# Kernel optimization log

Hardware: AMD Instinct MI355X
Metric: run time of the kernel (lower is better)

The kernel has to match this reference:

```python
import jax, jax.numpy as jnp
from jax import lax
import numpy as np

I_CNN = 2048   # box feature dim
Q_H = 1024     # LSTM hidden
Q_E = 300      # word embedding dim
HID = 512      # gated MLP hidden
B = 256
MAXN = 100
T = 14


def setup_inputs() -> dict:
    key = jax.random.key(0)
    ks = jax.random.split(key, 12)
    w = lambda k, shape: (jax.random.normal(k, shape, dtype=jnp.float32) * 0.02)
    return {
        "wholefeat": jax.random.normal(ks[0], (B, I_CNN), dtype=jnp.float32),
        "pooled": jax.random.normal(ks[1], (B, I_CNN), dtype=jnp.float32),
        "box_feats": jax.random.normal(ks[2], (B, MAXN, I_CNN), dtype=jnp.float32),
        "q_feats": jax.random.normal(ks[3], (B, T, Q_E), dtype=jnp.float32),
        "box_coords": jax.random.uniform(ks[4], (B, MAXN, 4), dtype=jnp.float32),
        "index": jax.random.randint(ks[5], (B,), 1, MAXN + 1),
        # LSTM params (PyTorch layout: gates ordered i,f,g,o)
        "W_ih": w(ks[6], (4 * Q_H, Q_E)),
        "W_hh": w(ks[7], (4 * Q_H, Q_H)),
        "b_ih": jnp.zeros((4 * Q_H,), jnp.float32),
        "b_hh": jnp.zeros((4 * Q_H,), jnp.float32),
        # gated MLP params
        "W_w": w(ks[8], (HID, I_CNN + Q_H)),
        "W_b": jnp.zeros((HID,), jnp.float32),
        "Wp_w": w(ks[9], (HID, I_CNN + Q_H)),
        "Wp_b": jnp.zeros((HID,), jnp.float32),
        "f_w": w(ks[10], (1, HID)),
    }


def _lstm_last(x_tbe, W_ih, W_hh, b_ih, b_hh):
    # x_tbe: [T, B, E] time-major. Returns final hidden state h_T: [B, H].
    H = W_hh.shape[1]
    # precompute input projections for all timesteps: [T, B, 4H]
    xg = jnp.einsum('tbe,ge->tbg', x_tbe, W_ih) + (b_ih + b_hh)

    def step(carry, xt):
        h, c = carry
        gates = xt + h @ W_hh.T                       # [B, 4H]
        i, f, g, o = jnp.split(gates, 4, axis=-1)
        i = jax.nn.sigmoid(i)
        f = jax.nn.sigmoid(f)
        g = jnp.tanh(g)
        o = jax.nn.sigmoid(o)
        c = f * c + i * g
        h = o * jnp.tanh(c)
        return (h, c), None

    h0 = jnp.zeros((x_tbe.shape[1], H), x_tbe.dtype)
    (h, _), _ = lax.scan(step, (h0, h0), xg)
    return h


def reference(wholefeat, pooled, box_feats, q_feats, box_coords, index,
              W_ih, W_hh, b_ih, b_hh, W_w, W_b, Wp_w, Wp_b, f_w):
    # question encoding: last LSTM output per sample -> [B, Q_H]
    q_rnn = _lstm_last(jnp.transpose(q_feats, (1, 0, 2)), W_ih, W_hh, b_ih, b_hh)

    Bn, N, _ = box_feats.shape
    qst = jnp.broadcast_to(q_rnn[:, None, :], (Bn, N, q_rnn.shape[-1]))
    b_full = jnp.concatenate([box_feats, qst], axis=-1)        # [B, N, 3072]

    y_tilde = jnp.tanh(jnp.einsum('bnd,hd->bnh', b_full, W_w) + W_b)
    g = jax.nn.sigmoid(jnp.einsum('bnd,hd->bnh', b_full, Wp_w) + Wp_b)
    si = y_tilde * g                                           # [B, N, HID]
    wsi = jax.nn.sigmoid(jnp.einsum('bnh,oh->bno', si, f_w))[..., 0]  # [B, N]

    # ragged reduction: only the first index[i] boxes of sample i contribute
    mask = (jnp.arange(N)[None, :] < index[:, None]).astype(wsi.dtype)
    return jnp.sum(wsi * mask, axis=1)                         # [B]
```

## Files before the change

kernel.cpp:

```cpp
#include <hip/hip_runtime.h>
#include <cstdint>
#include <cstddef>

#define DEVI __device__ __forceinline__

typedef __attribute__((ext_vector_type(8))) short short8;
typedef __attribute__((ext_vector_type(4))) float f32x4;
typedef __bf16 bf16x8 __attribute__((ext_vector_type(8)));

DEVI float sigf(float x) { return 1.0f / (1.0f + __expf(-x)); }
DEVI float tanh_f(float x) { return 2.0f / (1.0f + __expf(-2.0f * x)) - 1.0f; }

DEVI short f2bf(float x) {
    uint32_t u = __builtin_bit_cast(uint32_t, x);
    u += 0x7FFFu + ((u >> 16) & 1u);
    return (short)(u >> 16);
}
DEVI float bf2f(short s) {
    uint32_t u = ((uint32_t)(unsigned short)s) << 16;
    return __builtin_bit_cast(float, u);
}

DEVI void gload16(const void* g, void* l) {
    __builtin_amdgcn_global_load_lds(
        (const __attribute__((address_space(1))) void*)g,
        (__attribute__((address_space(3))) void*)l, 16, 0, 0);
}

DEVI f32x4 mfma16(short8 a, short8 b, f32x4 c) {
    return __builtin_amdgcn_mfma_f32_16x16x32_bf16(
        __builtin_bit_cast(bf16x8, a), __builtin_bit_cast(bf16x8, b), c, 0, 0, 0);
}


#define W_SLOTS   688128
#define WC_SLOTS  393216
#define XB_SLOTS  143360
#define HB_SLOTS  32768
#define C_SLOTS   65536
#define LG_SLOTS  6400
#define PREP_TOT  (W_SLOTS + WC_SLOTS + XB_SLOTS + HB_SLOTS + C_SLOTS + LG_SLOTS)

__global__ __launch_bounds__(256) void prep_all(const float* __restrict__ Wih,
                                                const float* __restrict__ Whh,
                                                const float* __restrict__ bih,
                                                const float* __restrict__ bhh,
                                                const float* __restrict__ Ww,
                                                const float* __restrict__ Wpw,
                                                const float* __restrict__ q,
                                                short* __restrict__ Wstk,
                                                short* __restrict__ Wcat,
                                                short* __restrict__ xb,
                                                short* __restrict__ hb0,
                                                float* __restrict__ c,
                                                float* __restrict__ lgt) {
    int s = blockIdx.x * 256 + threadIdx.x;
    if (s < W_SLOTS) {
        int n = s / 168, c8 = s - n * 168, kb = c8 * 8;
        int hblk = n >> 6, gate = (n >> 4) & 3, hl = n & 15;
        int on = gate * 1024 + hblk * 16 + hl;
        short8 o;
#pragma unroll
        for (int e = 0; e < 8; ++e) {
            int k = kb + e;
            float v;
            if (k < 300) v = Wih[on * 300 + k];
            else if (k == 300) v = bih[on] + bhh[on];
            else if (k < 320) v = 0.f;
            else v = Whh[on * 1024 + (k - 320)];
            o[e] = f2bf(v);
        }
        *(short8*)&Wstk[n * 1344 + kb] = o;
        return;
    }
    s -= W_SLOTS;
    if (s < WC_SLOTS) {
        int n = s / 384, c8 = s - n * 384, kb = c8 * 8;
        int hg = n >> 5, which = (n >> 4) & 1, hl = n & 15;
        int h = hg * 16 + hl;
        const float* src = (which ? Wpw : Ww) + (size_t)h * 3072 + kb;
        float4 v0 = *(const float4*)src;
        float4 v1 = *(const float4*)(src + 4);
        short8 o;
        o[0] = f2bf(v0.x); o[1] = f2bf(v0.y); o[2] = f2bf(v0.z); o[3] = f2bf(v0.w);
        o[4] = f2bf(v1.x); o[5] = f2bf(v1.y); o[6] = f2bf(v1.z); o[7] = f2bf(v1.w);
        *(short8*)&Wcat[(size_t)n * 3072 + kb] = o;
        return;
    }
    s -= WC_SLOTS;
    if (s < XB_SLOTS) {
        int row = s / 40, c8 = s - row * 40, eb = c8 * 8;
        int t = row / 256, b = row - t * 256;
        const float* qr = q + (size_t)(b * 14 + t) * 300;
        short8 o;
#pragma unroll
        for (int e = 0; e < 8; ++e) {
            int ee = eb + e;
            float v = (ee < 300) ? qr[ee] : (ee == 300 ? 1.0f : 0.0f);
            o[e] = f2bf(v);
        }
        *(short8*)&xb[(size_t)row * 320 + eb] = o;
        return;
    }
    s -= XB_SLOTS;
    if (s < HB_SLOTS) { ((short8*)hb0)[s] = short8{0,0,0,0,0,0,0,0}; return; }
    s -= HB_SLOTS;
    if (s < C_SLOTS) { ((f32x4*)c)[s] = f32x4{0.f,0.f,0.f,0.f}; return; }
    s -= C_SLOTS;
    if (s < LG_SLOTS) { ((f32x4*)lgt)[s] = f32x4{0.f,0.f,0.f,0.f}; return; }
}

__global__ __launch_bounds__(256) void prep_index(const int* __restrict__ index,
                                                  int* __restrict__ cum,
                                                  int* __restrict__ bmap) {
    __shared__ int s[256];
    int t = threadIdx.x;
    int myidx = index[t];
    s[t] = myidx;
    __syncthreads();
    for (int off = 1; off < 256; off <<= 1) {
        int v = (t >= off) ? s[t - off] : 0;
        __syncthreads();
        s[t] += v;
        __syncthreads();
    }
    cum[t + 1] = s[t];
    if (t == 0) cum[0] = 0;
    int base = s[t] - myidx;
    for (int j = 0; j < myidx; ++j) bmap[base + j] = t;
    int Ml = s[255];
    if (t < 128) bmap[Ml + t] = 0;
}

__global__ __launch_bounds__(256) void compact_box(const float* __restrict__ box,
                                                   const int* __restrict__ index,
                                                   const int* __restrict__ cum,
                                                   short* __restrict__ Ac) {
    int m = blockIdx.x;
    int b = m / 100, j = m - b * 100;
    if (j >= index[b]) return;
    size_t dr = (size_t)(cum[b] + j);
    int t = threadIdx.x;
    const float* src = box + (size_t)m * 2048 + t * 8;
    float4 v0 = *(const float4*)src;
    float4 v1 = *(const float4*)(src + 4);
    short8 s;
    s[0] = f2bf(v0.x); s[1] = f2bf(v0.y); s[2] = f2bf(v0.z); s[3] = f2bf(v0.w);
    s[4] = f2bf(v1.x); s[5] = f2bf(v1.y); s[6] = f2bf(v1.z); s[7] = f2bf(v1.w);
    *(short8*)&Ac[dr * 2048 + t * 8] = s;
}


__global__ __launch_bounds__(256) void xg_gemm(const short* __restrict__ xb,
                                               const short* __restrict__ Wstk,
                                               short* __restrict__ xg) {
    __shared__ __attribute__((aligned(16))) short As[128 * 64];
    __shared__ __attribute__((aligned(16))) short Bs[128 * 64];
    const int tid = threadIdx.x, l = tid & 63, w = tid >> 6;
    const int n0 = blockIdx.x * 128;
    const int m0 = blockIdx.y * 128;
    const int wm = w >> 1, wn = w & 1;

    const short* asrc[4];
    const short* bsrc[4];
    for (int i = 0; i < 4; i++) {
        int r = w * 32 + i * 8 + (l >> 3);
        int cs = (l & 7) ^ (r & 7);
        asrc[i] = xb + (size_t)(m0 + r) * 320 + cs * 8;
        bsrc[i] = Wstk + (size_t)(n0 + r) * 1344 + cs * 8;
    }

    f32x4 acc[4][4];
    for (int i = 0; i < 4; i++)
        for (int j = 0; j < 4; j++) acc[i][j] = f32x4{0.f, 0.f, 0.f, 0.f};

    for (int kt = 0; kt < 5; ++kt) {
        const int k0 = kt * 64;
        __syncthreads();
        for (int i = 0; i < 4; i++)
            gload16(asrc[i] + k0, &As[(w * 32 + i * 8) * 64]);
        for (int i = 0; i < 4; i++)
            gload16(bsrc[i] + k0, &Bs[(w * 32 + i * 8) * 64]);
        __syncthreads();
        for (int ks = 0; ks < 2; ++ks) {
            short8 a[4], b[4];
            for (int mf = 0; mf < 4; ++mf) {
                int m = wm * 64 + mf * 16 + (l & 15);
                int ca = (ks * 4 + (l >> 4)) ^ (m & 7);
                a[mf] = *(const short8*)&As[m * 64 + ca * 8];
            }
            for (int nf = 0; nf < 4; ++nf) {
                int n = wn * 64 + nf * 16 + (l & 15);
                int cb = (ks * 4 + (l >> 4)) ^ (n & 7);
                b[nf] = *(const short8*)&Bs[n * 64 + cb * 8];
            }
            for (int mf = 0; mf < 4; ++mf)
                for (int nf = 0; nf < 4; ++nf)
                    acc[mf][nf] = mfma16(a[mf], b[nf], acc[mf][nf]);
        }
    }
    const int hl = l & 15, hi = l >> 4;
    for (int mf = 0; mf < 4; ++mf)
        for (int nf = 0; nf < 4; ++nf)
            for (int rg = 0; rg < 4; ++rg) {
                int row = m0 + wm * 64 + mf * 16 + hi * 4 + rg;
                int col = n0 + wn * 64 + nf * 16 + hl;
                xg[(size_t)row * 4096 + col] = f2bf(acc[mf][nf][rg]);
            }
}


__global__ __launch_bounds__(128) void lstm_step(const short* __restrict__ hin,
                                                 const short* __restrict__ Wstk,
                                                 const short* __restrict__ xg_t,
                                                 float* __restrict__ c,
                                                 short* __restrict__ hout,
                                                 int dogemm) {
    __shared__ __attribute__((aligned(16))) short As[2][32 * 128];
    __shared__ __attribute__((aligned(16))) short Bs[2][64 * 128];
    const int tid = threadIdx.x, l = tid & 63, w = tid >> 6;
    const int hi = l >> 4, hl = l & 15;
    const int bid = blockIdx.x;
    const int xcd = bid & 7, ii = bid >> 3;
    const int ny = xcd * 8 + (ii & 7);
    const int mx = ii >> 3;
    const int m0 = mx * 32, n0g = ny * 64;

    f32x4 acc[4];
    for (int i = 0; i < 4; i++) acc[i] = f32x4{0.f, 0.f, 0.f, 0.f};

    if (dogemm) {
        const short* asrc[4];
        const short* bsrc[8];
        for (int i = 0; i < 4; i++) {
            int s = i * 128 + tid;
            int r = s >> 4, cs = s & 15;
            asrc[i] = hin + (size_t)(m0 + r) * 1024 + ((cs ^ (r & 15)) * 8);
        }
        for (int i = 0; i < 8; i++) {
            int s = i * 128 + tid;
            int r = s >> 4, cs = s & 15;
            bsrc[i] = Wstk + (size_t)(n0g + r) * 1344 + 320 + ((cs ^ (r & 15)) * 8);
        }
        for (int i = 0; i < 4; i++) gload16(asrc[i], &As[0][(i * 128 + tid) * 8]);
        for (int i = 0; i < 8; i++) gload16(bsrc[i], &Bs[0][(i * 128 + tid) * 8]);

        for (int kt = 0; kt < 8; ++kt) {
            const int cur = kt & 1;
            if (kt < 7) {
                const int k0 = (kt + 1) * 128;
                for (int i = 0; i < 4; i++)
                    gload16(asrc[i] + k0, &As[cur ^ 1][(i * 128 + tid) * 8]);
                for (int i = 0; i < 8; i++)
                    gload16(bsrc[i] + k0, &Bs[cur ^ 1][(i * 128 + tid) * 8]);
                asm volatile("s_waitcnt vmcnt(12)" ::: "memory");
            } else {
                asm volatile("s_waitcnt vmcnt(0)" ::: "memory");
            }
            __builtin_amdgcn_sched_barrier(0);
            __builtin_amdgcn_s_barrier();
            __builtin_amdgcn_sched_barrier(0);
#pragma unroll
            for (int ks = 0; ks < 4; ++ks) {
                const int mrow = w * 16 + hl;
                const int ca = (ks * 4 + hi) ^ hl;
                short8 a = *(const short8*)&As[cur][mrow * 128 + ca * 8];
#pragma unroll
                for (int nf = 0; nf < 4; ++nf) {
                    const int nrow = nf * 16 + hl;
                    short8 b = *(const short8*)&Bs[cur][nrow * 128 + ca * 8];
                    acc[nf] = mfma16(a, b, acc[nf]);
                }
            }
            __builtin_amdgcn_sched_barrier(0);
            asm volatile("s_waitcnt lgkmcnt(0)" ::: "memory");
            __builtin_amdgcn_s_barrier();
            __builtin_amdgcn_sched_barrier(0);
        }
    }

    const short* xr0 = xg_t + (size_t)(m0 + w * 16 + hi * 4) * 4096 + n0g + hl;
    for (int rg = 0; rg < 4; ++rg) {
        const short* xr = xr0 + (size_t)rg * 4096;
        float ig = acc[0][rg] + bf2f(xr[0]);
        float fg = acc[1][rg] + bf2f(xr[16]);
        float gg = acc[2][rg] + bf2f(xr[32]);
        float og = acc[3][rg] + bf2f(xr[48]);
        size_t off = (size_t)(m0 + w * 16 + hi * 4 + rg) * 1024 + ny * 16 + hl;
        float cn = sigf(fg) * c[off] + sigf(ig) * tanh_f(gg);
        c[off] = cn;
        hout[off] = f2bf(sigf(og) * tanh_f(cn));
    }
}


__global__ __launch_bounds__(256) void mlp_gemm(const short* __restrict__ Ac,
                                                const short* __restrict__ hb,
                                                const short* __restrict__ Wcat,
                                                const int* __restrict__ mliveptr,
                                                const int* __restrict__ bmap,
                                                const float* __restrict__ Wb,
                                                const float* __restrict__ Wpb,
                                                const float* __restrict__ fw,
                                                float* __restrict__ logits) {
    __shared__ __attribute__((aligned(16))) short As[2][128 * 64];
    __shared__ __attribute__((aligned(16))) short Bs[2][128 * 64];
    const int Mlive = *mliveptr;
    const int tid = threadIdx.x, l = tid & 63, w = tid >> 6;
    const int bid = blockIdx.x;
    const int xcd = bid & 7, ii = bid >> 3;
    const int x = ii & 7, q = ii >> 3;
    const int y = q * 8 + xcd;
    const int n0 = x * 128, m0 = y * 128;
    if (m0 >= Mlive) return;
    const int wm = w >> 1, wn = w & 1;

    const short* asrc[4];
    const short* hsrc[4];
    const short* bsrc[4];
    int ldso[4];
    for (int i = 0; i < 4; i++) {
        int r = w * 32 + i * 8 + (l >> 3);
        int cs = (l & 7) ^ (r & 7);
        asrc[i] = Ac + (size_t)(m0 + r) * 2048 + cs * 8;
        hsrc[i] = hb + (size_t)bmap[m0 + r] * 1024 + cs * 8;
        bsrc[i] = Wcat + (size_t)(n0 + r) * 3072 + cs * 8;
        ldso[i] = (w * 32 + i * 8) * 64;
    }

    f32x4 acc[4][4];
    for (int i = 0; i < 4; i++)
        for (int j = 0; j < 4; j++) acc[i][j] = f32x4{0.f, 0.f, 0.f, 0.f};

    for (int i = 0; i < 4; i++) gload16(asrc[i], &As[0][ldso[i]]);
    for (int i = 0; i < 4; i++) gload16(bsrc[i], &Bs[0][ldso[i]]);

    for (int kt = 0; kt < 48; ++kt) {
        const int cur = kt & 1;
        if (kt < 47) {
            const int k1 = (kt + 1) * 64;
            if (kt + 1 < 32) {
                for (int i = 0; i < 4; i++)
                    gload16(asrc[i] + k1, &As[cur ^ 1][ldso[i]]);
            } else {
                const int kq = k1 - 2048;
                for (int i = 0; i < 4; i++)
                    gload16(hsrc[i] + kq, &As[cur ^ 1][ldso[i]]);
            }
            for (int i = 0; i < 4; i++)
                gload16(bsrc[i] + k1, &Bs[cur ^ 1][ldso[i]]);
            asm volatile("s_waitcnt vmcnt(8)" ::: "memory");
        } else {
            asm volatile("s_waitcnt vmcnt(0)" ::: "memory");
        }
        __builtin_amdgcn_sched_barrier(0);
        __builtin_amdgcn_s_barrier();
        __builtin_amdgcn_sched_barrier(0);
        for (int ks = 0; ks < 2; ++ks) {
            short8 a[4], b[4];
            for (int mf = 0; mf < 4; ++mf) {
                int m = wm * 64 + mf * 16 + (l & 15);
                int ca = (ks * 4 + (l >> 4)) ^ (m & 7);
                a[mf] = *(const short8*)&As[cur][m * 64 + ca * 8];
            }
            for (int nf = 0; nf < 4; ++nf) {
                int n = wn * 64 + nf * 16 + (l & 15);
                int cb = (ks * 4 + (l >> 4)) ^ (n & 7);
                b[nf] = *(const short8*)&Bs[cur][n * 64 + cb * 8];
            }
            for (int mf = 0; mf < 4; ++mf)
                for (int nf = 0; nf < 4; ++nf)
                    acc[mf][nf] = mfma16(a[mf], b[nf], acc[mf][nf]);
        }
        __builtin_amdgcn_sched_barrier(0);
        asm volatile("s_waitcnt lgkmcnt(0)" ::: "memory");
        __builtin_amdgcn_s_barrier();
        __builtin_amdgcn_sched_barrier(0);
    }

    const int hl = l & 15, hi = l >> 4;
    for (int mf = 0; mf < 4; ++mf) {
        float part[4] = {0.f, 0.f, 0.f, 0.f};
        for (int p = 0; p < 2; ++p) {
            int ntg = (n0 + wn * 64) / 16 + 2 * p;
            int hg = ntg >> 1;
            int h = hg * 16 + hl;
            float fwv = fw[h], wbv = Wb[h], wpbv = Wpb[h];
            for (int rg = 0; rg < 4; ++rg) {
                float y2 = tanh_f(acc[mf][2 * p][rg] + wbv);
                float g2 = sigf(acc[mf][2 * p + 1][rg] + wpbv);
                part[rg] += y2 * g2 * fwv;
            }
        }
        for (int rg = 0; rg < 4; ++rg) {
            float v = part[rg];
            v += __shfl_xor(v, 1, 64);
            v += __shfl_xor(v, 2, 64);
            v += __shfl_xor(v, 4, 64);
            v += __shfl_xor(v, 8, 64);
            if (hl == 0) {
                int row = m0 + wm * 64 + mf * 16 + hi * 4 + rg;
                atomicAdd(&logits[row], v);
            }
        }
    }
}

__global__ __launch_bounds__(128) void reduce_out(const float* __restrict__ logits,
                                                  const int* __restrict__ index,
                                                  const int* __restrict__ cum,
                                                  float* __restrict__ out) {
    int b = blockIdx.x, t = threadIdx.x;
    int idx = index[b];
    int base = cum[b];
    float v = 0.f;
    if (t < 100 && t < idx) v = sigf(logits[base + t]);
    for (int m = 32; m; m >>= 1) v += __shfl_down(v, m, 64);
    __shared__ float s[2];
    if ((t & 63) == 0) s[t >> 6] = v;
    __syncthreads();
    if (t == 0) out[b] = s[0] + s[1];
}


extern "C" void kernel_launch(void* const* d_in, const int* in_sizes, int n_in,
                              void* d_out, int out_size, void* d_ws, size_t ws_size,
                              hipStream_t stream) {
    (void)in_sizes; (void)n_in; (void)out_size; (void)ws_size;
    const float* box = (const float*)d_in[2];
    const float* qf  = (const float*)d_in[3];
    const int* index = (const int*)d_in[5];
    const float* Wih = (const float*)d_in[6];
    const float* Whh = (const float*)d_in[7];
    const float* bih = (const float*)d_in[8];
    const float* bhh = (const float*)d_in[9];
    const float* Ww  = (const float*)d_in[10];
    const float* Wb  = (const float*)d_in[11];
    const float* Wpw = (const float*)d_in[12];
    const float* Wpb = (const float*)d_in[13];
    const float* fw  = (const float*)d_in[14];

    char* p = (char*)d_ws;
    short* Wstk = (short*)p;  p += (size_t)4096 * 1344 * 2;
    short* Wcat = (short*)p;  p += (size_t)1024 * 3072 * 2;
    short* xb   = (short*)p;  p += (size_t)3584 * 320 * 2;
    short* hb0  = (short*)p;  p += (size_t)256 * 1024 * 2;
    short* hb1  = (short*)p;  p += (size_t)256 * 1024 * 2;
    short* xg   = (short*)p;  p += (size_t)3584 * 4096 * 2;
    float* c    = (float*)p;  p += (size_t)256 * 1024 * 4;
    int*   cum  = (int*)p;    p += 260 * 4;
    int*   bmap = (int*)p;    p += (size_t)(25600 + 128) * 4;
    float* lgt  = (float*)p;  p += (size_t)25600 * 4;
    p = (char*)(((uintptr_t)p + 255) & ~(uintptr_t)255);
    short* Ac   = (short*)p;  p += (size_t)25600 * 2048 * 2;

    prep_index<<<1, 256, 0, stream>>>(index, cum, bmap);
    prep_all<<<(PREP_TOT + 255) / 256, 256, 0, stream>>>(
        Wih, Whh, bih, bhh, Ww, Wpw, qf, Wstk, Wcat, xb, hb0, c, lgt);

    compact_box<<<25600, 256, 0, stream>>>(box, index, cum, Ac);

    xg_gemm<<<dim3(32, 28), 256, 0, stream>>>(xb, Wstk, xg);

    short* hbuf[2] = {hb0, hb1};
    for (int t = 0; t < 14; ++t) {
        lstm_step<<<512, 128, 0, stream>>>(
            hbuf[t & 1], Wstk, xg + (size_t)t * 256 * 4096, c,
            hbuf[(t & 1) ^ 1], t == 0 ? 0 : 1);
    }

    mlp_gemm<<<1600, 256, 0, stream>>>(Ac, hb0, Wcat, cum + 256, bmap,
                                       Wb, Wpb, fw, lgt);
    reduce_out<<<256, 128, 0, stream>>>(lgt, index, cum, (float*)d_out);
}
```

Baseline: 341.1 us.

## Fuse prep kernels, fold LSTM step 0 into xg_gemm, retile MLP GEMM

The index prefix-scan now runs as block 0 of prep_all, and the zero-init of h0 and c is dropped. The first LSTM step, where h0 is zero, is computed in the xg_gemm epilogue, which writes c and h1 directly and removes one lstm_step launch. mlp_gemm switches to 512-thread blocks with 256-row M tiles and single-buffered LDS with __syncthreads, replacing the double-buffered prefetch pipeline. This halves the block count but loses load/compute overlap inside each block, relying on more waves per block to hide latency instead.

```diff
diff --git a/kernel.cpp b/kernel.cpp
--- a/kernel.cpp
+++ b/kernel.cpp
@@ -36,25 +36,43 @@
 #define W_SLOTS   688128
 #define WC_SLOTS  393216
 #define XB_SLOTS  143360
-#define HB_SLOTS  32768
-#define C_SLOTS   65536
 #define LG_SLOTS  6400
-#define PREP_TOT  (W_SLOTS + WC_SLOTS + XB_SLOTS + HB_SLOTS + C_SLOTS + LG_SLOTS)
-
-__global__ __launch_bounds__(256) void prep_all(const float* __restrict__ Wih,
+#define PREP_TOT  (W_SLOTS + WC_SLOTS + XB_SLOTS + LG_SLOTS)
+
+__global__ __launch_bounds__(256) void prep_all(const int* __restrict__ index,
+                                                const float* __restrict__ Wih,
                                                 const float* __restrict__ Whh,
                                                 const float* __restrict__ bih,
                                                 const float* __restrict__ bhh,
                                                 const float* __restrict__ Ww,
                                                 const float* __restrict__ Wpw,
                                                 const float* __restrict__ q,
+                                                int* __restrict__ cum,
+                                                int* __restrict__ bmap,
                                                 short* __restrict__ Wstk,
                                                 short* __restrict__ Wcat,
                                                 short* __restrict__ xb,
-                                                short* __restrict__ hb0,
-                                                float* __restrict__ c,
                                                 float* __restrict__ lgt) {
-    int s = blockIdx.x * 256 + threadIdx.x;
+    __shared__ int sh[256];
+    if (blockIdx.x == 0) {
+        int t = threadIdx.x;
+        int myidx = index[t];
+        sh[t] = myidx;
+        __syncthreads();
+        for (int off = 1; off < 256; off <<= 1) {
+            int v = (t >= off) ? sh[t - off] : 0;
+            __syncthreads();
+            sh[t] += v;
+            __syncthreads();
+        }
+        cum[t + 1] = sh[t];
+        if (t == 0) cum[0] = 0;
+        int base = sh[t] - myidx;
+        for (int j = 0; j < myidx; ++j) bmap[base + j] = t;
+        bmap[sh[255] + t] = 0;
+        return;
+    }
+    int s = (blockIdx.x - 1) * 256 + threadIdx.x;
     if (s < W_SLOTS) {
         int n = s / 168, c8 = s - n * 168, kb = c8 * 8;
         int hblk = n >> 6, gate = (n >> 4) & 3, hl = n & 15;
@@ -103,33 +121,7 @@
         return;
     }
     s -= XB_SLOTS;
-    if (s < HB_SLOTS) { ((short8*)hb0)[s] = short8{0,0,0,0,0,0,0,0}; return; }
-    s -= HB_SLOTS;
-    if (s < C_SLOTS) { ((f32x4*)c)[s] = f32x4{0.f,0.f,0.f,0.f}; return; }
-    s -= C_SLOTS;
-    if (s < LG_SLOTS) { ((f32x4*)lgt)[s] = f32x4{0.f,0.f,0.f,0.f}; return; }
-}
-
-__global__ __launch_bounds__(256) void prep_index(const int* __restrict__ index,
-                                                  int* __restrict__ cum,
-                                                  int* __restrict__ bmap) {
-    __shared__ int s[256];
-    int t = threadIdx.x;
-    int myidx = index[t];
-    s[t] = myidx;
-    __syncthreads();
-    for (int off = 1; off < 256; off <<= 1) {
-        int v = (t >= off) ? s[t - off] : 0;
-        __syncthreads();
-        s[t] += v;
-        __syncthreads();
-    }
-    cum[t + 1] = s[t];
-    if (t == 0) cum[0] = 0;
-    int base = s[t] - myidx;
-    for (int j = 0; j < myidx; ++j) bmap[base + j] = t;
-    int Ml = s[255];
-    if (t < 128) bmap[Ml + t] = 0;
+    if (s < LG_SLOTS) { ((f32x4*)lgt)[s] = f32x4{0.f, 0.f, 0.f, 0.f}; return; }
 }
 
 __global__ __launch_bounds__(256) void compact_box(const float* __restrict__ box,
@@ -153,7 +145,9 @@
 
 __global__ __launch_bounds__(256) void xg_gemm(const short* __restrict__ xb,
                                                const short* __restrict__ Wstk,
-                                               short* __restrict__ xg) {
+                                               short* __restrict__ xg,
+                                               float* __restrict__ c,
+                                               short* __restrict__ hb1) {
     __shared__ __attribute__((aligned(16))) short As[128 * 64];
     __shared__ __attribute__((aligned(16))) short Bs[128 * 64];
     const int tid = threadIdx.x, l = tid & 63, w = tid >> 6;
@@ -200,13 +194,28 @@
         }
     }
     const int hl = l & 15, hi = l >> 4;
-    for (int mf = 0; mf < 4; ++mf)
-        for (int nf = 0; nf < 4; ++nf)
+    if (m0 < 256) {
+        const int h = ((n0 + wn * 64) >> 6) * 16 + hl;
+        for (int mf = 0; mf < 4; ++mf)
             for (int rg = 0; rg < 4; ++rg) {
-                int row = m0 + wm * 64 + mf * 16 + hi * 4 + rg;
-                int col = n0 + wn * 64 + nf * 16 + hl;
-                xg[(size_t)row * 4096 + col] = f2bf(acc[mf][nf][rg]);
-            }
+                int b = m0 + wm * 64 + mf * 16 + hi * 4 + rg;
+                float ig = acc[mf][0][rg];
+                float gg = acc[mf][2][rg];
+                float og = acc[mf][3][rg];
+                float cn = sigf(ig) * tanh_f(gg);
+                size_t off = (size_t)b * 1024 + h;
+                c[off] = cn;
+                hb1[off] = f2bf(sigf(og) * tanh_f(cn));
+            }
+    } else {
+        for (int mf = 0; mf < 4; ++mf)
+            for (int nf = 0; nf < 4; ++nf)
+                for (int rg = 0; rg < 4; ++rg) {
+                    int row = m0 + wm * 64 + mf * 16 + hi * 4 + rg;
+                    int col = n0 + wn * 64 + nf * 16 + hl;
+                    xg[(size_t)row * 4096 + col] = f2bf(acc[mf][nf][rg]);
+                }
+    }
 }
 
 
@@ -214,8 +223,7 @@
                                                  const short* __restrict__ Wstk,
                                                  const short* __restrict__ xg_t,
                                                  float* __restrict__ c,
-                                                 short* __restrict__ hout,
-                                                 int dogemm) {
+                                                 short* __restrict__ hout) {
     __shared__ __attribute__((aligned(16))) short As[2][32 * 128];
     __shared__ __attribute__((aligned(16))) short Bs[2][64 * 128];
     const int tid = threadIdx.x, l = tid & 63, w = tid >> 6;
@@ -229,54 +237,52 @@
     f32x4 acc[4];
     for (int i = 0; i < 4; i++) acc[i] = f32x4{0.f, 0.f, 0.f, 0.f};
 
-    if (dogemm) {
-        const short* asrc[4];
-        const short* bsrc[8];
-        for (int i = 0; i < 4; i++) {
-            int s = i * 128 + tid;
-            int r = s >> 4, cs = s & 15;
-            asrc[i] = hin + (size_t)(m0 + r) * 1024 + ((cs ^ (r & 15)) * 8);
-        }
-        for (int i = 0; i < 8; i++) {
-            int s = i * 128 + tid;
-            int r = s >> 4, cs = s & 15;
-            bsrc[i] = Wstk + (size_t)(n0g + r) * 1344 + 320 + ((cs ^ (r & 15)) * 8);
-        }
-        for (int i = 0; i < 4; i++) gload16(asrc[i], &As[0][(i * 128 + tid) * 8]);
-        for (int i = 0; i < 8; i++) gload16(bsrc[i], &Bs[0][(i * 128 + tid) * 8]);
-
-        for (int kt = 0; kt < 8; ++kt) {
-            const int cur = kt & 1;
-            if (kt < 7) {
-                const int k0 = (kt + 1) * 128;
-                for (int i = 0; i < 4; i++)
-                    gload16(asrc[i] + k0, &As[cur ^ 1][(i * 128 + tid) * 8]);
-                for (int i = 0; i < 8; i++)
-                    gload16(bsrc[i] + k0, &Bs[cur ^ 1][(i * 128 + tid) * 8]);
-                asm volatile("s_waitcnt vmcnt(12)" ::: "memory");
-            } else {
-                asm volatile("s_waitcnt vmcnt(0)" ::: "memory");
-            }
-            __builtin_amdgcn_sched_barrier(0);
-            __builtin_amdgcn_s_barrier();
-            __builtin_amdgcn_sched_barrier(0);
+    const short* asrc[4];
+    const short* bsrc[8];
+    for (int i = 0; i < 4; i++) {
+        int s = i * 128 + tid;
+        int r = s >> 4, cs = s & 15;
+        asrc[i] = hin + (size_t)(m0 + r) * 1024 + ((cs ^ (r & 15)) * 8);
+    }
+    for (int i = 0; i < 8; i++) {
+        int s = i * 128 + tid;
+        int r = s >> 4, cs = s & 15;
+        bsrc[i] = Wstk + (size_t)(n0g + r) * 1344 + 320 + ((cs ^ (r & 15)) * 8);
+    }
+    for (int i = 0; i < 4; i++) gload16(asrc[i], &As[0][(i * 128 + tid) * 8]);
+    for (int i = 0; i < 8; i++) gload16(bsrc[i], &Bs[0][(i * 128 + tid) * 8]);
+
+    for (int kt = 0; kt < 8; ++kt) {
+        const int cur = kt & 1;
+        if (kt < 7) {
+            const int k0 = (kt + 1) * 128;
+            for (int i = 0; i < 4; i++)
+                gload16(asrc[i] + k0, &As[cur ^ 1][(i * 128 + tid) * 8]);
+            for (int i = 0; i < 8; i++)
+                gload16(bsrc[i] + k0, &Bs[cur ^ 1][(i * 128 + tid) * 8]);
+            asm volatile("s_waitcnt vmcnt(12)" ::: "memory");
+        } else {
+            asm volatile("s_waitcnt vmcnt(0)" ::: "memory");
+        }
+        __builtin_amdgcn_sched_barrier(0);
+        __builtin_amdgcn_s_barrier();
+        __builtin_amdgcn_sched_barrier(0);
 #pragma unroll
-            for (int ks = 0; ks < 4; ++ks) {
-                const int mrow = w * 16 + hl;
-                const int ca = (ks * 4 + hi) ^ hl;
-                short8 a = *(const short8*)&As[cur][mrow * 128 + ca * 8];
+        for (int ks = 0; ks < 4; ++ks) {
+            const int mrow = w * 16 + hl;
+            const int ca = (ks * 4 + hi) ^ hl;
+            short8 a = *(const short8*)&As[cur][mrow * 128 + ca * 8];
 #pragma unroll
-                for (int nf = 0; nf < 4; ++nf) {
-                    const int nrow = nf * 16 + hl;
-                    short8 b = *(const short8*)&Bs[cur][nrow * 128 + ca * 8];
-                    acc[nf] = mfma16(a, b, acc[nf]);
-                }
-            }
-            __builtin_amdgcn_sched_barrier(0);
-            asm volatile("s_waitcnt lgkmcnt(0)" ::: "memory");
-            __builtin_amdgcn_s_barrier();
-            __builtin_amdgcn_sched_barrier(0);
-        }
+            for (int nf = 0; nf < 4; ++nf) {
+                const int nrow = nf * 16 + hl;
+                short8 b = *(const short8*)&Bs[cur][nrow * 128 + ca * 8];
+                acc[nf] = mfma16(a, b, acc[nf]);
+            }
+        }
+        __builtin_amdgcn_sched_barrier(0);
+        asm volatile("s_waitcnt lgkmcnt(0)" ::: "memory");
+        __builtin_amdgcn_s_barrier();
+        __builtin_amdgcn_sched_barrier(0);
     }
 
     const short* xr0 = xg_t + (size_t)(m0 + w * 16 + hi * 4) * 4096 + n0g + hl;
@@ -294,7 +300,7 @@
 }
 
 
-__global__ __launch_bounds__(256) void mlp_gemm(const short* __restrict__ Ac,
+__global__ __launch_bounds__(512) void mlp_gemm(const short* __restrict__ Ac,
                                                 const short* __restrict__ hb,
                                                 const short* __restrict__ Wcat,
                                                 const int* __restrict__ mliveptr,
@@ -303,79 +309,71 @@
                                                 const float* __restrict__ Wpb,
                                                 const float* __restrict__ fw,
                                                 float* __restrict__ logits) {
-    __shared__ __attribute__((aligned(16))) short As[2][128 * 64];
-    __shared__ __attribute__((aligned(16))) short Bs[2][128 * 64];
+    __shared__ __attribute__((aligned(16))) short As[256 * 64];
+    __shared__ __attribute__((aligned(16))) short Bs[128 * 64];
     const int Mlive = *mliveptr;
     const int tid = threadIdx.x, l = tid & 63, w = tid >> 6;
     const int bid = blockIdx.x;
     const int xcd = bid & 7, ii = bid >> 3;
     const int x = ii & 7, q = ii >> 3;
     const int y = q * 8 + xcd;
-    const int n0 = x * 128, m0 = y * 128;
+    const int n0 = x * 128, m0 = y * 256;
     if (m0 >= Mlive) return;
     const int wm = w >> 1, wn = w & 1;
 
     const short* asrc[4];
     const short* hsrc[4];
-    const short* bsrc[4];
-    int ldso[4];
+    int adst[4];
+    const short* bsrc[2];
+    int bdst[2];
     for (int i = 0; i < 4; i++) {
-        int r = w * 32 + i * 8 + (l >> 3);
+        int r = i * 64 + w * 8 + (l >> 3);
         int cs = (l & 7) ^ (r & 7);
         asrc[i] = Ac + (size_t)(m0 + r) * 2048 + cs * 8;
         hsrc[i] = hb + (size_t)bmap[m0 + r] * 1024 + cs * 8;
+        adst[i] = (i * 64 + w * 8) * 64;
+    }
+    for (int i = 0; i < 2; i++) {
+        int r = i * 64 + w * 8 + (l >> 3);
+        int cs = (l & 7) ^ (r & 7);
         bsrc[i] = Wcat + (size_t)(n0 + r) * 3072 + cs * 8;
-        ldso[i] = (w * 32 + i * 8) * 64;
+        bdst[i] = (i * 64 + w * 8) * 64;
     }
 
     f32x4 acc[4][4];
     for (int i = 0; i < 4; i++)
         for (int j = 0; j < 4; j++) acc[i][j] = f32x4{0.f, 0.f, 0.f, 0.f};
 
-    for (int i = 0; i < 4; i++) gload16(asrc[i], &As[0][ldso[i]]);
-    for (int i = 0; i < 4; i++) gload16(bsrc[i], &Bs[0][ldso[i]]);
-
     for (int kt = 0; kt < 48; ++kt) {
-        const int cur = kt & 1;
-        if (kt < 47) {
-            const int k1 = (kt + 1) * 64;
-            if (kt + 1 < 32) {
-                for (int i = 0; i < 4; i++)
-                    gload16(asrc[i] + k1, &As[cur ^ 1][ldso[i]]);
-            } else {
-                const int kq = k1 - 2048;
-                for (int i = 0; i < 4; i++)
-                    gload16(hsrc[i] + kq, &As[cur ^ 1][ldso[i]]);
-            }
+        const int k0 = kt * 64;
+        __syncthreads();
+        if (kt < 32) {
             for (int i = 0; i < 4; i++)
-                gload16(bsrc[i] + k1, &Bs[cur ^ 1][ldso[i]]);
-            asm volatile("s_waitcnt vmcnt(8)" ::: "memory");
+                gload16(asrc[i] + k0, &As[adst[i]]);
         } else {
-            asm volatile("s_waitcnt vmcnt(0)" ::: "memory");
-        }
-        __builtin_amdgcn_sched_barrier(0);
-        __builtin_amdgcn_s_barrier();
-        __builtin_amdgcn_sched_barrier(0);
+            const int kq = k0 - 2048;
+            for (int i = 0; i < 4; i++)
+                gload16(hsrc[i] + kq, &As[adst[i]]);
+        }
+        for (int i = 0; i < 2; i++)
+            gload16(bsrc[i] + k0, &Bs[bdst[i]]);
+        __syncthreads();
         for (int ks = 0; ks < 2; ++ks) {
             short8 a[4], b[4];
             for (int mf = 0; mf < 4; ++mf) {
                 int m = wm * 64 + mf * 16 + (l & 15);
                 int ca = (ks * 4 + (l >> 4)) ^ (m & 7);
-                a[mf] = *(const short8*)&As[cur][m * 64 + ca * 8];
+                a[mf] = *(const short8*)&As[m * 64 + ca * 8];
             }
             for (int nf = 0; nf < 4; ++nf) {
                 int n = wn * 64 + nf * 16 + (l & 15);
                 int cb = (ks * 4 + (l >> 4)) ^ (n & 7);
-                b[nf] = *(const short8*)&Bs[cur][n * 64 + cb * 8];
+                b[nf] = *(const short8*)&Bs[n * 64 + cb * 8];
             }
             for (int mf = 0; mf < 4; ++mf)
                 for (int nf = 0; nf < 4; ++nf)
                     acc[mf][nf] = mfma16(a[mf], b[nf], acc[mf][nf]);
         }
-        __builtin_amdgcn_sched_barrier(0);
-        asm volatile("s_waitcnt lgkmcnt(0)" ::: "memory");
-        __builtin_amdgcn_s_barrier();
-        __builtin_amdgcn_sched_barrier(0);
     }
 
     const int hl = l & 15, hi = l >> 4;
@@ -449,27 +447,25 @@
     short* xg   = (short*)p;  p += (size_t)3584 * 4096 * 2;
     float* c    = (float*)p;  p += (size_t)256 * 1024 * 4;
     int*   cum  = (int*)p;    p += 260 * 4;
-    int*   bmap = (int*)p;    p += (size_t)(25600 + 128) * 4;
+    int*   bmap = (int*)p;    p += (size_t)(25600 + 256) * 4;
     float* lgt  = (float*)p;  p += (size_t)25600 * 4;
     p = (char*)(((uintptr_t)p + 255) & ~(uintptr_t)255);
     short* Ac   = (short*)p;  p += (size_t)25600 * 2048 * 2;
 
-    prep_index<<<1, 256, 0, stream>>>(index, cum, bmap);
-    prep_all<<<(PREP_TOT + 255) / 256, 256, 0, stream>>>(
-        Wih, Whh, bih, bhh, Ww, Wpw, qf, Wstk, Wcat, xb, hb0, c, lgt);
+    prep_all<<<1 + PREP_TOT / 256, 256, 0, stream>>>(
+        index, Wih, Whh, bih, bhh, Ww, Wpw, qf, cum, bmap, Wstk, Wcat, xb, lgt);
 
     compact_box<<<25600, 256, 0, stream>>>(box, index, cum, Ac);
 
-    xg_gemm<<<dim3(32, 28), 256, 0, stream>>>(xb, Wstk, xg);
+    xg_gemm<<<dim3(32, 28), 256, 0, stream>>>(xb, Wstk, xg, c, hb1);
 
     short* hbuf[2] = {hb0, hb1};
-    for (int t = 0; t < 14; ++t) {
+    for (int t = 1; t < 14; ++t) {
         lstm_step<<<512, 128, 0, stream>>>(
-            hbuf[t & 1], Wstk, xg + (size_t)t * 256 * 4096, c,
-            hbuf[(t & 1) ^ 1], t == 0 ? 0 : 1);
-    }
-
-    mlp_gemm<<<1600, 256, 0, stream>>>(Ac, hb0, Wcat, cum + 256, bmap,
-                                       Wb, Wpb, fw, lgt);
+            hbuf[t & 1], Wstk, xg + (size_t)t * 256 * 4096, c, hbuf[(t & 1) ^ 1]);
+    }
+
+    mlp_gemm<<<800, 512, 0, stream>>>(Ac, hb0, Wcat, cum + 256, bmap,
+                                      Wb, Wpb, fw, lgt);
     reduce_out<<<256, 128, 0, stream>>>(lgt, index, cum, (float*)d_out);
 }
```

Result: faster. 299.0 us (-12.3%).
